# Performance work log

Hardware: AMD Instinct MI355X
Metric: run time of the kernel (lower is better)

Reference implementation:

```python
import jax, jax.numpy as jnp
import numpy as np


def lstm_cell(x, h, c, Wi, Wh, b):
    # PyTorch LSTMCell gate order: i, f, g, o
    g = x @ Wi.T + h @ Wh.T + b
    i, f, gg, o = jnp.split(g, 4, axis=-1)
    c = jax.nn.sigmoid(f) * c + jax.nn.sigmoid(i) * jnp.tanh(gg)
    h = jax.nn.sigmoid(o) * jnp.tanh(c)
    return h, c


def setup_inputs() -> dict:
    key = jax.random.key(0)
    ks = jax.random.split(key, 32)
    S, B, L, N, T = 20, 16, 30, 6, 20
    H, E, Vs, Vt = 512, 512, 50000, 30000
    w = lambda k, shape: jax.random.normal(k, shape, jnp.float32) * 0.05
    return {
        'articles': jax.random.randint(ks[0], (S, B, L), 0, Vs, jnp.int32),
        'summaries': jax.random.randint(ks[1], (N, B, T), 0, Vt, jnp.int32),
        'emb_src': w(ks[2], (Vs, E)),
        'emb_tgt': w(ks[3], (Vt, E)),
        'we_Wi': w(ks[4], (4 * H, E)), 'we_Wh': w(ks[5], (4 * H, H)), 'we_b': w(ks[6], (4 * H,)),
        'se_Wi': w(ks[7], (4 * H, H)), 'se_Wh': w(ks[8], (4 * H, H)), 'se_b': w(ks[9], (4 * H,)),
        'W_feat': w(ks[10], (H, H)), 'b_feat': w(ks[11], (H,)),
        'wd_Wi': w(ks[12], (4 * H, E)), 'wd_Wh': w(ks[13], (4 * H, H)), 'wd_b': w(ks[14], (4 * H,)),
        'W_vocab': w(ks[15], (Vt, H)), 'b_vocab': w(ks[16], (Vt,)),
        'sd_Wi': w(ks[17], (4 * H, H)), 'sd_Wh': w(ks[18], (4 * H, H)), 'sd_b': w(ks[19], (4 * H,)),
        'attn_Wh': w(ks[20], (H, H)), 'attn_wc': w(ks[21], (H,)), 'attn_v': w(ks[22], (H,)),
        'W_out': w(ks[23], (H, 2 * H)), 'b_out': w(ks[24], (H,)),
    }


def _forward(articles, summaries, emb_src, emb_tgt, we_Wi, we_Wh, we_b,
             se_Wi, se_Wh, se_b, W_feat, b_feat, wd_Wi, wd_Wh, wd_b,
             W_vocab, b_vocab, sd_Wi, sd_Wh, sd_b, attn_Wh, attn_wc, attn_v,
             W_out, b_out):
    S, B, L = articles.shape
    H = we_Wh.shape[1]

    # ---- word encoder: LSTMCell over each sentence, vmapped over S ----
    def encode_sentence(tokens):  # [B, L]
        x = emb_src[tokens]  # [B, L, E]
        z = jnp.zeros((B, H), x.dtype)
        def step(hc, xt):
            h, c = lstm_cell(xt, hc[0], hc[1], we_Wi, we_Wh, we_b)
            return (h, c), None
        (h, _), _ = jax.lax.scan(step, (z, z), jnp.swapaxes(x, 0, 1))
        return h
    word_hx = jax.vmap(encode_sentence)(articles)  # [S, B, H]

    # ---- sentence encoder: LSTM over sentence dim ----
    z = jnp.zeros((B, H), word_hx.dtype)
    def senc_step(hc, x):
        h, c = lstm_cell(x, hc[0], hc[1], se_Wi, se_Wh, se_b)
        return (h, c), h
    (s_hx, s_cx), sent_out = jax.lax.scan(senc_step, (z, z), word_hx)  # sent_out [S,B,H]
    sent_feat = sent_out @ W_feat.T + b_feat  # precomputed attention features

    mask = (articles[:, :, 0:1] > 0).astype(jnp.float32)  # [S, B, 1]
    coverage0 = jnp.zeros_like(mask)

    # ---- hierarchical decoder over summary sentences ----
    def sent_step(carry, sent):  # sent [B, T]
        w_hx, w_cx, s_hx, s_cx, coverage, loss = carry
        seq = sent.T  # [T, B]

        def word_step(wc, ba):
            wh, wcell, l = wc
            wb, wa = ba
            wh, wcell = lstm_cell(emb_tgt[wb], wh, wcell, wd_Wi, wd_Wh, wd_b)
            logits = wh @ W_vocab.T + b_vocab  # [B, V]
            logp = jax.nn.log_softmax(logits, axis=-1)
            nll = -jnp.take_along_axis(logp, wa[:, None], axis=1)[:, 0]
            m = (wa != 0).astype(logits.dtype)  # ignore_index=0
            l = l + jnp.sum(nll * m) / jnp.maximum(jnp.sum(m), 1.0)
            return (wh, wcell, l), None

        (w_hx, w_cx, loss), _ = jax.lax.scan(word_step, (w_hx, w_cx, loss), (seq[:-1], seq[1:]))

        # sentence decoder step with coverage attention over S sentences
        s_h2, s_cx = lstm_cell(w_hx, s_hx, s_cx, sd_Wi, sd_Wh, sd_b)
        e = jnp.einsum('sbh,h->sb', jnp.tanh(sent_feat + s_h2 @ attn_Wh.T + coverage * attn_wc), attn_v)
        e = jnp.where(mask[:, :, 0] > 0, e, -1e9)
        align = jax.nn.softmax(e, axis=0)[:, :, None]  # [S, B, 1]
        context = jnp.sum(align * sent_out, axis=0)  # [B, H]
        final = jnp.tanh(jnp.concatenate([context, s_h2], axis=-1) @ W_out.T + b_out)
        # coverage loss (with pre-update coverage), then accumulate coverage
        loss = loss + jnp.mean(jnp.sum(jnp.minimum(align[:, :, 0], coverage[:, :, 0]), axis=0))
        coverage = coverage + align
        return (final, w_cx, final, s_cx, coverage, loss), None

    init = (s_hx, s_cx, s_hx, s_cx, coverage0, jnp.float32(0.0))
    (_, _, _, _, _, loss), _ = jax.lax.scan(sent_step, init, summaries)
    return loss


def reference(articles, summaries, emb_src, emb_tgt, we_Wi, we_Wh, we_b,
              se_Wi, se_Wh, se_b, W_feat, b_feat, wd_Wi, wd_Wh, wd_b,
              W_vocab, b_vocab, sd_Wi, sd_Wh, sd_b, attn_Wh, attn_wc, attn_v,
              W_out, b_out):
    return _forward(articles, summaries, emb_src, emb_tgt, we_Wi, we_Wh, we_b,
                    se_Wi, se_Wh, se_b, W_feat, b_feat, wd_Wi, wd_Wh, wd_b,
                    W_vocab, b_vocab, sd_Wi, sd_Wh, sd_b, attn_Wh, attn_wc,
                    attn_v, W_out, b_out)
```

## Files before the change

### kernel.cpp

```cpp
#include <hip/hip_runtime.h>
#include <cstdint>
#include <cstddef>

#define H 512
#define SS 20
#define BB 16
#define LL 30
#define NN 6
#define TT 20
#define VT 30000
#define MROWS 1824
#define NSTEPS 114
#define MPAD 1856
#define NT2 120
#define UBLK 16
#define NV 232
#define MEGA 248

#define SCOPE_AGENT __HIP_MEMORY_SCOPE_AGENT

typedef __attribute__((ext_vector_type(8))) short bf16x8;
typedef __attribute__((ext_vector_type(4))) float f32x4;

__device__ __forceinline__ float sigmoidf_(float x) { return 1.f / (1.f + expf(-x)); }
__device__ __forceinline__ float b2f(ushort u) { return __uint_as_float(((uint32_t)u) << 16); }
__device__ __forceinline__ ushort f2b_rne(float f) {
  uint32_t u = __float_as_uint(f);
  return (ushort)((u + 0x7fffu + ((u >> 16) & 1u)) >> 16);
}

__device__ __forceinline__ void ast_u32(uint* p, uint v) {
  __hip_atomic_store(p, v, __ATOMIC_RELAXED, SCOPE_AGENT);
}
__device__ __forceinline__ uint ald_u32(const uint* p) {
  return __hip_atomic_load(p, __ATOMIC_RELAXED, SCOPE_AGENT);
}

__device__ __forceinline__ void sbar(uint* flags, int slot, int nblk, uint phase)
{
  __syncthreads();
  if (threadIdx.x == 0) {
    __builtin_amdgcn_fence(__ATOMIC_RELEASE, "agent");
    ast_u32(&flags[slot * 16], phase);
  }
  if ((int)threadIdx.x < nblk) {
    while (ald_u32(&flags[threadIdx.x * 16]) < phase)
      __builtin_amdgcn_s_sleep(1);
  }
  __syncthreads();
  if (threadIdx.x == 0)
    __builtin_amdgcn_fence(__ATOMIC_ACQUIRE, "agent");
  __syncthreads();
}

struct PrepP {
  const int* articles; const int* summaries;
  const float* emb_src; const float* emb_tgt;
  const float* we_Wi; const float* wd_Wi; const float* we_Wh;
  const float* se_Wi; const float* se_Wh; const float* W_feat;
  const float* wd_Wh; const float* sd_Wi; const float* sd_Wh;
  const float* attn_Wh; const float* W_out;
  ushort* A_we; ushort* A_wd;
  ushort* weWi; ushort* wdWi; ushort* weWh;
  ushort* seWi; ushort* seWh; ushort* wfeat;
  ushort* wdWh; ushort* sdWi; ushort* sdWh;
  ushort* attnWh; ushort* Wout;
};

__device__ __forceinline__ void conv_f2b(const float* __restrict__ src,
                                         ushort* __restrict__ dst, int n4,
                                         int t0, int stride)
{
  for (int i = t0; i < n4; i += stride) {
    float4 v = reinterpret_cast<const float4*>(src)[i];
    ushort4 o;
    o.x = f2b_rne(v.x); o.y = f2b_rne(v.y);
    o.z = f2b_rne(v.z); o.w = f2b_rne(v.w);
    reinterpret_cast<ushort4*>(dst)[i] = o;
  }
}

__global__ __launch_bounds__(256) void prep_kernel(PrepP P)
{
  const int t0 = blockIdx.x * 256 + threadIdx.x;
  const int stride = gridDim.x * 256;
  for (int i = t0; i < SS * BB * LL * H; i += stride) {
    int m = i >> 9, k = i & 511;
    int l = m / (SS * BB), sb = m % (SS * BB);
    int tok = P.articles[sb * LL + l];
    P.A_we[i] = f2b_rne(P.emb_src[(size_t)tok * H + k]);
  }
  for (int i = t0; i < MROWS * H; i += stride) {
    int m = i >> 9, k = i & 511;
    int stp = m >> 4, b = m & 15;
    int n = stp / (TT - 1), t = stp % (TT - 1);
    int tok = P.summaries[(n * BB + b) * TT + t];
    P.A_wd[i] = f2b_rne(P.emb_tgt[(size_t)tok * H + k]);
  }
  const int Q = 4 * H * H / 4;
  conv_f2b(P.we_Wi, P.weWi, Q, t0, stride);
  conv_f2b(P.wd_Wi, P.wdWi, Q, t0, stride);
  conv_f2b(P.we_Wh, P.weWh, Q, t0, stride);
  conv_f2b(P.se_Wi, P.seWi, Q, t0, stride);
  conv_f2b(P.se_Wh, P.seWh, Q, t0, stride);
  conv_f2b(P.wd_Wh, P.wdWh, Q, t0, stride);
  conv_f2b(P.sd_Wi, P.sdWi, Q, t0, stride);
  conv_f2b(P.sd_Wh, P.sdWh, Q, t0, stride);
  conv_f2b(P.W_feat, P.wfeat, H * H / 4, t0, stride);
  conv_f2b(P.attn_Wh, P.attnWh, H * H / 4, t0, stride);
  conv_f2b(P.W_out, P.Wout, H * 2 * H / 4, t0, stride);
}

__global__ __launch_bounds__(512) void proj_mfma_kernel(
    const ushort* __restrict__ A_we, const ushort* __restrict__ weWi,
    const float* __restrict__ we_b, ushort* __restrict__ XiW,
    const ushort* __restrict__ A_wd, const ushort* __restrict__ wdWi,
    const float* __restrict__ wd_b, ushort* __restrict__ XiD)
{
  int bid = blockIdx.x;
  const ushort* A; const ushort* W; const float* bias; ushort* C; int M, mt, nt;
  if (bid < 1200) { A = A_we; W = weWi; bias = we_b; C = XiW; M = 9600; mt = bid >> 3; nt = bid & 7; }
  else { int b2 = bid - 1200; A = A_wd; W = wdWi; bias = wd_b; C = XiD; M = MROWS; mt = b2 >> 3; nt = b2 & 7; }
  const int tid = threadIdx.x, wid = tid >> 6, lane = tid & 63;
  const int wm = wid >> 2, wn = wid & 3;
  const int m0 = mt * 64 + wm * 32, n0 = nt * 256 + wn * 64;
  const int lr = lane & 15, lk = (lane >> 4) << 3;

  f32x4 acc[2][4];
#pragma unroll
  for (int i = 0; i < 2; ++i)
#pragma unroll
    for (int nf = 0; nf < 4; ++nf) acc[i][nf] = (f32x4)0.0f;

  for (int k0 = 0; k0 < H; k0 += 32) {
    bf16x8 a[2], b[4];
#pragma unroll
    for (int i = 0; i < 2; ++i) {
      int m = m0 + i * 16 + lr;
      bf16x8 az = (bf16x8)(short)0;
      if (m < M) az = *reinterpret_cast<const bf16x8*>(A + (size_t)m * H + k0 + lk);
      a[i] = az;
    }
#pragma unroll
    for (int nf = 0; nf < 4; ++nf)
      b[nf] = *reinterpret_cast<const bf16x8*>(W + (size_t)(n0 + nf * 16 + lr) * H + k0 + lk);
#pragma unroll
    for (int i = 0; i < 2; ++i)
#pragma unroll
      for (int nf = 0; nf < 4; ++nf)
        acc[i][nf] = __builtin_amdgcn_mfma_f32_16x16x32_bf16(a[i], b[nf], acc[i][nf], 0, 0, 0);
  }
#pragma unroll
  for (int i = 0; i < 2; ++i)
#pragma unroll
    for (int nf = 0; nf < 4; ++nf) {
      int n = n0 + nf * 16 + lr;
      float bv = bias[n];
#pragma unroll
      for (int jreg = 0; jreg < 4; ++jreg) {
        int row = m0 + i * 16 + (lane >> 4) * 4 + jreg;
        if (row < M) C[(size_t)row * 2048 + n] = f2b_rne(acc[i][nf][jreg] + bv);
      }
    }
}

struct MP {
  const ushort* XiW; const ushort* XiD;
  const ushort* weWh; const ushort* seWi; const ushort* seWh;
  const ushort* wfeat; const ushort* wdWh; const ushort* sdWi;
  const ushort* sdWh; const ushort* attnWh; const ushort* Wout;
  const float* se_b; const float* b_feat; const float* sd_b; const float* b_out;
  const float* attn_wc; const float* attn_v; const int* articles;
  ushort* h0; ushort* h1;
  float* XiS;
  ushort* sh0; ushort* sh1;
  float* sent_out; ushort* sent_out_bf; float* sent_feat;
  ushort* wh_bf; ushort* sdh_bf; ushort* final_bf; ushort* catb;
  float* qb; float* loss;
  uint* sflags;
  uint* vbflags;
  uint* vflag;
  const float* Wv; ushort* Wv_bf; const float* bv; float* partials;
};

__global__ __launch_bounds__(512) void mega_kernel(MP P)
{
  const int tid = threadIdx.x, bid = blockIdx.x;
  const int wid = tid >> 6, lane = tid & 63;
  const int lr = lane & 15;
  const int lk = (lane >> 4) << 3;
  const int orow = (lane >> 4) << 2;

  const bool isSeq = (bid < 128) && ((bid & 7) == 0);

  if (!isSeq) {
    const int v = (bid < 128) ? (bid - (bid >> 3) - 1) : (bid - UBLK);
    const int mt = v >> 3, chunk = v & 7;
    __shared__ float red[4][64][2];

    if (tid == 0) {
      while (ald_u32(P.vflag) < 1u) __builtin_amdgcn_s_sleep(16);
    }
    __syncthreads();
    {
      const int n4 = VT * H / 4;
      for (int i = v * 512 + tid; i < n4; i += NV * 512) {
        float4 w = reinterpret_cast<const float4*>(P.Wv)[i];
        ushort4 o;
        o.x = f2b_rne(w.x); o.y = f2b_rne(w.y);
        o.z = f2b_rne(w.z); o.w = f2b_rne(w.w);
        reinterpret_cast<ushort4*>(P.Wv_bf)[i] = o;
      }
    }
    sbar(P.vbflags, v, NV, 1u);

    {
      int lastStep = mt * 4 + 3; if (lastStep > NSTEPS - 1) lastStep = NSTEPS - 1;
      uint want = 2u + (uint)(lastStep / (TT - 1));
      if (tid == 0) {
        while (ald_u32(P.vflag) < want) __builtin_amdgcn_s_sleep(16);
        __builtin_amdgcn_fence(__ATOMIC_ACQUIRE, "agent");
      }
      __syncthreads();
    }

    const int wm = wid >> 2, wn = wid & 3;
    const int m0 = mt * 64 + wm * 32;
    bf16x8 areg[2][16];
#pragma unroll
    for (int i = 0; i < 2; ++i)
#pragma unroll
      for (int kk = 0; kk < 16; ++kk)
        areg[i][kk] = *reinterpret_cast<const bf16x8*>(
            P.wh_bf + (size_t)(m0 + i * 16 + lr) * H + kk * 32 + lk);

    for (int nt2 = 0; nt2 < 15; ++nt2) {
      const int n0 = chunk * 3840 + nt2 * 256 + wn * 64;
      f32x4 acc[2][4];
#pragma unroll
      for (int i = 0; i < 2; ++i)
#pragma unroll
        for (int nf = 0; nf < 4; ++nf) acc[i][nf] = (f32x4)0.0f;

#pragma unroll 4
      for (int kk = 0; kk < 16; ++kk) {
        bf16x8 b[4];
#pragma unroll
        for (int nf = 0; nf < 4; ++nf) {
          int n = n0 + nf * 16 + lr;
          bf16x8 bz = (bf16x8)(short)0;
          if (n < VT) bz = *reinterpret_cast<const bf16x8*>(P.Wv_bf + (size_t)n * H + kk * 32 + lk);
          b[nf] = bz;
        }
#pragma unroll
        for (int i = 0; i < 2; ++i)
#pragma unroll
          for (int nf = 0; nf < 4; ++nf)
            acc[i][nf] = __builtin_amdgcn_mfma_f32_16x16x32_bf16(areg[i][kk], b[nf], acc[i][nf], 0, 0, 0);
      }

      float bc[4];
      int val[4];
#pragma unroll
      for (int nf = 0; nf < 4; ++nf) {
        int n = n0 + nf * 16 + lr;
        val[nf] = (n < VT);
        bc[nf] = val[nf] ? P.bv[n] : 0.f;
      }
#pragma unroll
      for (int i = 0; i < 2; ++i) {
#pragma unroll
        for (int jreg = 0; jreg < 4; ++jreg) {
          float lg[4];
          float mx = -3.0e38f;
#pragma unroll
          for (int nf = 0; nf < 4; ++nf) {
            lg[nf] = val[nf] ? (acc[i][nf][jreg] + bc[nf]) : -3.0e38f;
            mx = fmaxf(mx, lg[nf]);
          }
#pragma unroll
          for (int d = 1; d < 16; d <<= 1) mx = fmaxf(mx, __shfl_xor(mx, d));
          float s = 0.f;
#pragma unroll
          for (int nf = 0; nf < 4; ++nf) s += val[nf] ? expf(lg[nf] - mx) : 0.f;
#pragma unroll
          for (int d = 1; d < 16; d <<= 1) s += __shfl_xor(s, d);
          if (lr == 0) {
            int rloc = wm * 32 + i * 16 + (lane >> 4) * 4 + jreg;
            red[wn][rloc][0] = mx;
            red[wn][rloc][1] = s;
          }
        }
      }
      __syncthreads();
      if (tid < 64) {
        int r2 = tid;
        float M = -3.0e38f;
#pragma unroll
        for (int q = 0; q < 4; ++q) M = fmaxf(M, red[q][r2][0]);
        float S = 0.f;
#pragma unroll
        for (int q = 0; q < 4; ++q) S += red[q][r2][1] * expf(red[q][r2][0] - M);
        size_t p = ((size_t)(mt * 64 + r2) * NT2 + chunk * 15 + nt2) * 2;
        P.partials[p] = M;
        P.partials[p + 1] = S;
      }
      __syncthreads();
    }
    return;
  }

  const int sid = bid >> 3;
  __shared__ f32x4 hred[2][4][64];
  __shared__ float e_l[SS], align_l[SS], cov_l[SS];
  const int gw = sid * 8 + wid;
  uint ph = 0;

  {
    float cst[5][4];
#pragma unroll
    for (int it = 0; it < 5; ++it)
#pragma unroll
      for (int rg = 0; rg < 4; ++rg) cst[it][rg] = 0.f;
    ushort* cur = P.h0;
    ushort* nxt = P.h1;
    const int ug = gw & 31;
    const int unit = ug * 16 + lr;
    const ushort* wb = P.weWh + (size_t)(ug * 16 + lr) * H + lk;
    for (int l = 0; l < LL; ++l) {
#pragma unroll
      for (int it = 0; it < 5; ++it) {
        int mt = (gw + it * 128) >> 5;
        f32x4 acc[4];
#pragma unroll
        for (int g = 0; g < 4; ++g) acc[g] = (f32x4)0.0f;
        const ushort* ab = cur + (size_t)(mt * 16 + lr) * H + lk;
#pragma unroll
        for (int k0 = 0; k0 < H; k0 += 32) {
          bf16x8 a = *reinterpret_cast<const bf16x8*>(ab + k0);
#pragma unroll
          for (int g = 0; g < 4; ++g) {
            bf16x8 b = *reinterpret_cast<const bf16x8*>(wb + (size_t)g * H * H + k0);
            acc[g] = __builtin_amdgcn_mfma_f32_16x16x32_bf16(a, b, acc[g], 0, 0, 0);
          }
        }
#pragma unroll
        for (int rg = 0; rg < 4; ++rg) {
          int row = mt * 16 + orow + rg;
          const ushort* xi = P.XiW + (size_t)(l * 320 + row) * 2048 + unit;
          float gi = acc[0][rg] + b2f(xi[0]);
          float gf = acc[1][rg] + b2f(xi[512]);
          float gc = acc[2][rg] + b2f(xi[1024]);
          float go = acc[3][rg] + b2f(xi[1536]);
          float c = sigmoidf_(gf) * cst[it][rg] + sigmoidf_(gi) * tanhf(gc);
          float h = sigmoidf_(go) * tanhf(c);
          cst[it][rg] = c;
          nxt[(size_t)row * H + unit] = f2b_rne(h);
        }
      }
      sbar(P.sflags, sid, UBLK, ++ph);
      ushort* t = cur; cur = nxt; nxt = t;
    }
    {
      const ushort* wbs = P.seWi + (size_t)(ug * 16 + lr) * H + lk;
#pragma unroll
      for (int it = 0; it < 5; ++it) {
        int mt = (gw + it * 128) >> 5;
        f32x4 acc[4];
#pragma unroll
        for (int g = 0; g < 4; ++g) acc[g] = (f32x4)0.0f;
        const ushort* ab = cur + (size_t)(mt * 16 + lr) * H + lk;
#pragma unroll
        for (int k0 = 0; k0 < H; k0 += 32) {
          bf16x8 a = *reinterpret_cast<const bf16x8*>(ab + k0);
#pragma unroll
          for (int g = 0; g < 4; ++g) {
            bf16x8 b = *reinterpret_cast<const bf16x8*>(wbs + (size_t)g * H * H + k0);
            acc[g] = __builtin_amdgcn_mfma_f32_16x16x32_bf16(a, b, acc[g], 0, 0, 0);
          }
        }
#pragma unroll
        for (int rg = 0; rg < 4; ++rg) {
          int row = mt * 16 + orow + rg;
#pragma unroll
          for (int g = 0; g < 4; ++g)
            P.XiS[(size_t)row * 2048 + g * H + unit] = acc[g][rg] + P.se_b[g * H + unit];
        }
      }
    }
    sbar(P.sflags, sid, UBLK, ++ph);
    if (sid == 0 && tid == 0)
      __hip_atomic_store(P.vflag, 1u, __ATOMIC_RELEASE, SCOPE_AGENT);
  }

  float cw[4] = {0.f, 0.f, 0.f, 0.f};
  float csd[4] = {0.f, 0.f, 0.f, 0.f};
  {
    float cse[4] = {0.f, 0.f, 0.f, 0.f};
    ushort* cur = P.sh0;
    ushort* nxt = P.sh1;
    const int ug = sid * 2 + wid;
    const int unit = ug * 16 + lr;
    for (int s = 0; s < SS; ++s) {
      if (wid < 2) {
        f32x4 acc[4];
#pragma unroll
        for (int g = 0; g < 4; ++g) acc[g] = (f32x4)0.0f;
        const ushort* ab = cur + (size_t)lr * H + lk;
        const ushort* wb = P.seWh + (size_t)(ug * 16 + lr) * H + lk;
#pragma unroll
        for (int k0 = 0; k0 < H; k0 += 32) {
          bf16x8 a = *reinterpret_cast<const bf16x8*>(ab + k0);
#pragma unroll
          for (int g = 0; g < 4; ++g) {
            bf16x8 b = *reinterpret_cast<const bf16x8*>(wb + (size_t)g * H * H + k0);
            acc[g] = __builtin_amdgcn_mfma_f32_16x16x32_bf16(a, b, acc[g], 0, 0, 0);
          }
        }
#pragma unroll
        for (int rg = 0; rg < 4; ++rg) {
          int row = orow + rg;
          const float* xi = P.XiS + (size_t)(s * 16 + row) * 2048 + unit;
          float gi = acc[0][rg] + xi[0];
          float gf = acc[1][rg] + xi[512];
          float gc = acc[2][rg] + xi[1024];
          float go = acc[3][rg] + xi[1536];
          float c = sigmoidf_(gf) * cse[rg] + sigmoidf_(gi) * tanhf(gc);
          float h = sigmoidf_(go) * tanhf(c);
          cse[rg] = c;
          nxt[(size_t)row * H + unit] = f2b_rne(h);
          P.sent_out[(size_t)(s * 16 + row) * H + unit] = h;
          P.sent_out_bf[(size_t)(s * 16 + row) * H + unit] = f2b_rne(h);
        }
      }
      sbar(P.sflags, sid, UBLK, ++ph);
      ushort* t = cur; cur = nxt; nxt = t;
    }
    if (wid < 2) {
      f32x4 v; v[0] = cse[0]; v[1] = cse[1]; v[2] = cse[2]; v[3] = cse[3];
      hred[wid][0][lane] = v;
#pragma unroll
      for (int rg = 0; rg < 4; ++rg) csd[rg] = cse[rg];
    }
    __syncthreads();
    if (wid < 4 && !(wid & 1)) {
      f32x4 v = hred[wid >> 1][0][lane];
      cw[0] = v[0]; cw[1] = v[1]; cw[2] = v[2]; cw[3] = v[3];
    }
    __syncthreads();
  }

  {
    const int ug = gw & 31;
    const int unit = ug * 16 + lr;
    const ushort* wb = P.wfeat + (size_t)(ug * 16 + lr) * H + lk;
#pragma unroll
    for (int it = 0; it < 5; ++it) {
      int mt = (gw + it * 128) >> 5;
      f32x4 acc = (f32x4)0.0f;
      const ushort* ab = P.sent_out_bf + (size_t)(mt * 16 + lr) * H + lk;
#pragma unroll
      for (int k0 = 0; k0 < H; k0 += 32) {
        bf16x8 a = *reinterpret_cast<const bf16x8*>(ab + k0);
        bf16x8 b = *reinterpret_cast<const bf16x8*>(wb + k0);
        acc = __builtin_amdgcn_mfma_f32_16x16x32_bf16(a, b, acc, 0, 0, 0);
      }
#pragma unroll
      for (int rg = 0; rg < 4; ++rg) {
        int row = mt * 16 + orow + rg;
        P.sent_feat[(size_t)row * H + unit] = acc[rg] + P.b_feat[unit];
      }
    }
    if (tid < SS) cov_l[tid] = 0.f;
    sbar(P.sflags, sid, UBLK, ++ph);
  }

  {
    const int half = wid & 1;
    const int ug2 = sid * 2 + (wid >> 1);
    const int unit2 = ug2 * 16 + lr;
    const int ug = sid * 2 + wid;
    const int unit = ug * 16 + lr;
    const int b_ = sid;

    for (int n = 0; n < NN; ++n) {
      bf16x8 wreg[4][8];
      if (wid < 4) {
#pragma unroll
        for (int g = 0; g < 4; ++g)
#pragma unroll
          for (int kk = 0; kk < 8; ++kk)
            wreg[g][kk] = *reinterpret_cast<const bf16x8*>(
                P.wdWh + (size_t)g * H * H + (size_t)(ug2 * 16 + lr) * H +
                half * 256 + kk * 32 + lk);
      }
      for (int t = 0; t < TT - 1; ++t) {
        int stp = n * (TT - 1) + t;
        f32x4 acc[4];
        if (wid < 4) {
          const ushort* A = (t == 0)
              ? ((n == 0) ? P.sh0 : P.final_bf)
              : P.wh_bf + (size_t)(stp - 1) * 16 * H;
#pragma unroll
          for (int g = 0; g < 4; ++g) acc[g] = (f32x4)0.0f;
          const ushort* ab = A + (size_t)lr * H + half * 256 + lk;
#pragma unroll
          for (int kk = 0; kk < 8; ++kk) {
            bf16x8 a = *reinterpret_cast<const bf16x8*>(ab + kk * 32);
#pragma unroll
            for (int g = 0; g < 4; ++g)
              acc[g] = __builtin_amdgcn_mfma_f32_16x16x32_bf16(a, wreg[g][kk], acc[g], 0, 0, 0);
          }
          if (half) {
#pragma unroll
            for (int g = 0; g < 4; ++g) hred[wid >> 1][g][lane] = acc[g];
          }
        }
        __syncthreads();
        if (wid < 4 && !half) {
#pragma unroll
          for (int g = 0; g < 4; ++g) acc[g] += hred[wid >> 1][g][lane];
#pragma unroll
          for (int rg = 0; rg < 4; ++rg) {
            int row = orow + rg;
            const ushort* xi = P.XiD + (size_t)(stp * 16 + row) * 2048 + unit2;
            float gi = acc[0][rg] + b2f(xi[0]);
            float gf = acc[1][rg] + b2f(xi[512]);
            float gc = acc[2][rg] + b2f(xi[1024]);
            float go = acc[3][rg] + b2f(xi[1536]);
            float c = sigmoidf_(gf) * cw[rg] + sigmoidf_(gi) * tanhf(gc);
            float h = sigmoidf_(go) * tanhf(c);
            cw[rg] = c;
            P.wh_bf[(size_t)(stp * 16 + row) * H + unit2] = f2b_rne(h);
          }
        }
        sbar(P.sflags, sid, UBLK, ++ph);
      }
      if (sid == 0 && tid == 0)
        __hip_atomic_store(P.vflag, 2u + (uint)n, __ATOMIC_RELEASE, SCOPE_AGENT);
      if (wid < 2) {
        f32x4 acc[4];
#pragma unroll
        for (int g = 0; g < 4; ++g) acc[g] = (f32x4)0.0f;
        const ushort* A1 = P.wh_bf + (size_t)(n * (TT - 1) + TT - 2) * 16 * H;
        const ushort* A2 = (n == 0) ? P.sh0 : P.final_bf;
        const ushort* ab1 = A1 + (size_t)lr * H + lk;
        const ushort* wb1 = P.sdWi + (size_t)(ug * 16 + lr) * H + lk;
#pragma unroll
        for (int k0 = 0; k0 < H; k0 += 32) {
          bf16x8 a = *reinterpret_cast<const bf16x8*>(ab1 + k0);
#pragma unroll
          for (int g = 0; g < 4; ++g) {
            bf16x8 b = *reinterpret_cast<const bf16x8*>(wb1 + (size_t)g * H * H + k0);
            acc[g] = __builtin_amdgcn_mfma_f32_16x16x32_bf16(a, b, acc[g], 0, 0, 0);
          }
        }
        const ushort* ab2 = A2 + (size_t)lr * H + lk;
        const ushort* wb2 = P.sdWh + (size_t)(ug * 16 + lr) * H + lk;
#pragma unroll
        for (int k0 = 0; k0 < H; k0 += 32) {
          bf16x8 a = *reinterpret_cast<const bf16x8*>(ab2 + k0);
#pragma unroll
          for (int g = 0; g < 4; ++g) {
            bf16x8 b = *reinterpret_cast<const bf16x8*>(wb2 + (size_t)g * H * H + k0);
            acc[g] = __builtin_amdgcn_mfma_f32_16x16x32_bf16(a, b, acc[g], 0, 0, 0);
          }
        }
#pragma unroll
        for (int rg = 0; rg < 4; ++rg) {
          int row = orow + rg;
          float gi = acc[0][rg] + P.sd_b[0 * H + unit];
          float gf = acc[1][rg] + P.sd_b[1 * H + unit];
          float gc = acc[2][rg] + P.sd_b[2 * H + unit];
          float go = acc[3][rg] + P.sd_b[3 * H + unit];
          float c = sigmoidf_(gf) * csd[rg] + sigmoidf_(gi) * tanhf(gc);
          float h = sigmoidf_(go) * tanhf(c);
          csd[rg] = c;
          P.sdh_bf[(size_t)row * H + unit] = f2b_rne(h);
        }
      }
      sbar(P.sflags, sid, UBLK, ++ph);
      if (wid < 2) {
        f32x4 acc = (f32x4)0.0f;
        const ushort* ab = P.sdh_bf + (size_t)lr * H + lk;
        const ushort* wb = P.attnWh + (size_t)(ug * 16 + lr) * H + lk;
#pragma unroll
        for (int k0 = 0; k0 < H; k0 += 32) {
          bf16x8 a = *reinterpret_cast<const bf16x8*>(ab + k0);
          bf16x8 b = *reinterpret_cast<const bf16x8*>(wb + k0);
          acc = __builtin_amdgcn_mfma_f32_16x16x32_bf16(a, b, acc, 0, 0, 0);
        }
#pragma unroll
        for (int rg = 0; rg < 4; ++rg)
          P.qb[(size_t)(orow + rg) * H + unit] = acc[rg];
      }
      sbar(P.sflags, sid, UBLK, ++ph);
      for (int s = wid; s < SS; s += 8) {
        float cov = cov_l[s];
        float sum = 0.f;
        for (int h2 = lane; h2 < H; h2 += 64)
          sum += tanhf(P.sent_feat[(size_t)(s * 16 + b_) * H + h2] +
                       P.qb[b_ * H + h2] + cov * P.attn_wc[h2]) * P.attn_v[h2];
#pragma unroll
        for (int d = 1; d < 64; d <<= 1) sum += __shfl_xor(sum, d);
        if (lane == 0)
          e_l[s] = (P.articles[(s * 16 + b_) * LL] > 0) ? sum : -1e9f;
      }
      __syncthreads();
      if (wid == 0) {
        float ev = (lane < SS) ? e_l[lane] : -3.0e38f;
        float mx = ev;
#pragma unroll
        for (int d = 1; d < 64; d <<= 1) mx = fmaxf(mx, __shfl_xor(mx, d));
        float ex = (lane < SS) ? expf(ev - mx) : 0.f;
        float s = ex;
#pragma unroll
        for (int d = 1; d < 64; d <<= 1) s += __shfl_xor(s, d);
        float al = ex / s;
        float cl = 0.f;
        if (lane < SS) {
          float cov = cov_l[lane];
          cl = fminf(al, cov);
          cov_l[lane] = cov + al;
          align_l[lane] = al;
        }
#pragma unroll
        for (int d = 1; d < 64; d <<= 1) cl += __shfl_xor(cl, d);
        if (lane == 0) atomicAdd(P.loss, cl * (1.f / BB));
      }
      __syncthreads();
      if (tid < 512) {
        float s = 0.f;
#pragma unroll
        for (int ss2 = 0; ss2 < SS; ++ss2)
          s += align_l[ss2] * P.sent_out[(size_t)(ss2 * 16 + b_) * H + tid];
        P.catb[b_ * 1024 + tid] = f2b_rne(s);
        P.catb[b_ * 1024 + 512 + tid] = P.sdh_bf[(size_t)b_ * H + tid];
      }
      sbar(P.sflags, sid, UBLK, ++ph);
      if (wid < 2) {
        f32x4 acc = (f32x4)0.0f;
        const ushort* ab = P.catb + (size_t)lr * 1024 + lk;
        const ushort* wb = P.Wout + (size_t)(ug * 16 + lr) * 1024 + lk;
#pragma unroll
        for (int k0 = 0; k0 < 1024; k0 += 32) {
          bf16x8 a = *reinterpret_cast<const bf16x8*>(ab + k0);
          bf16x8 b = *reinterpret_cast<const bf16x8*>(wb + k0);
          acc = __builtin_amdgcn_mfma_f32_16x16x32_bf16(a, b, acc, 0, 0, 0);
        }
#pragma unroll
        for (int rg = 0; rg < 4; ++rg) {
          int row = orow + rg;
          float v = tanhf(acc[rg] + P.b_out[unit]);
          P.final_bf[(size_t)row * H + unit] = f2b_rne(v);
        }
      }
      sbar(P.sflags, sid, UBLK, ++ph);
    }
    if (sid == 0 && tid == 0)
      __hip_atomic_store(P.vflag, 7u, __ATOMIC_RELEASE, SCOPE_AGENT);
  }
}

__global__ void tlog_kernel(const ushort* __restrict__ wh_bf,
                            const ushort* __restrict__ Wv_bf,
                            const float* __restrict__ bv,
                            const int* __restrict__ summaries,
                            float* __restrict__ tlog)
{
  int row = blockIdx.x;
  int lane = threadIdx.x;
  int b = row & 15, stp = row >> 4;
  int n = stp / (TT - 1), t = stp % (TT - 1);
  int tgt = summaries[(n * BB + b) * TT + t + 1];
  float s = 0.f;
  for (int k = lane; k < H; k += 64)
    s += b2f(wh_bf[(size_t)row * H + k]) * b2f(Wv_bf[(size_t)tgt * H + k]);
#pragma unroll
  for (int d = 1; d < 64; d <<= 1) s += __shfl_xor(s, d);
  if (lane == 0) tlog[row] = s + bv[tgt];
}

__global__ __launch_bounds__(256) void nll_kernel(
    const float* __restrict__ partials, const float* __restrict__ tlog,
    const int* __restrict__ summaries, float* __restrict__ loss)
{
  int stp = blockIdx.x;
  int tid = threadIdx.x;
  int rr = tid >> 4, ch = tid & 15;
  int row = stp * 16 + rr;
  const float* pr = partials + (size_t)row * NT2 * 2;
  float mx = -3.0e38f;
  for (int t2 = ch; t2 < NT2; t2 += 16) mx = fmaxf(mx, pr[t2 * 2]);
#pragma unroll
  for (int d = 1; d < 16; d <<= 1) mx = fmaxf(mx, __shfl_xor(mx, d));
  float s = 0.f;
  for (int t2 = ch; t2 < NT2; t2 += 16) s += pr[t2 * 2 + 1] * expf(pr[t2 * 2] - mx);
#pragma unroll
  for (int d = 1; d < 16; d <<= 1) s += __shfl_xor(s, d);
  __shared__ float sh_n[16], sh_m[16];
  if (ch == 0) {
    float lse = mx + logf(s);
    float nll = lse - tlog[row];
    int b = row & 15;
    int n = stp / (TT - 1), t = stp % (TT - 1);
    int wa = summaries[(n * BB + b) * TT + t + 1];
    sh_n[rr] = (wa != 0) ? nll : 0.f;
    sh_m[rr] = (wa != 0) ? 1.f : 0.f;
  }
  __syncthreads();
  if (tid == 0) {
    float sn = 0.f, sm = 0.f;
    for (int r2 = 0; r2 < 16; ++r2) { sn += sh_n[r2]; sm += sh_m[r2]; }
    atomicAdd(loss, sn / fmaxf(sm, 1.f));
  }
}

extern "C" void kernel_launch(void* const* d_in, const int* in_sizes, int n_in,
                              void* d_out, int out_size, void* d_ws, size_t ws_size,
                              hipStream_t stream)
{
  (void)in_sizes; (void)n_in; (void)out_size; (void)ws_size;
  const int*   articles  = (const int*)d_in[0];
  const int*   summaries = (const int*)d_in[1];
  const float* emb_src   = (const float*)d_in[2];
  const float* emb_tgt   = (const float*)d_in[3];
  const float* we_Wi = (const float*)d_in[4];
  const float* we_Wh = (const float*)d_in[5];
  const float* we_b  = (const float*)d_in[6];
  const float* se_Wi = (const float*)d_in[7];
  const float* se_Wh = (const float*)d_in[8];
  const float* se_b  = (const float*)d_in[9];
  const float* W_feat = (const float*)d_in[10];
  const float* b_feat = (const float*)d_in[11];
  const float* wd_Wi = (const float*)d_in[12];
  const float* wd_Wh = (const float*)d_in[13];
  const float* wd_b  = (const float*)d_in[14];
  const float* W_vocab = (const float*)d_in[15];
  const float* b_vocab = (const float*)d_in[16];
  const float* sd_Wi = (const float*)d_in[17];
  const float* sd_Wh = (const float*)d_in[18];
  const float* sd_b  = (const float*)d_in[19];
  const float* attn_Wh = (const float*)d_in[20];
  const float* attn_wc = (const float*)d_in[21];
  const float* attn_v  = (const float*)d_in[22];
  const float* W_out = (const float*)d_in[23];
  const float* b_out = (const float*)d_in[24];

  char* wsb = (char*)d_ws;
  size_t off = 0;
  auto alloc = [&](size_t bytes) -> char* {
    char* p = wsb + off;
    off += (bytes + 255) & ~(size_t)255;
    return p;
  };

  char* regA = alloc(9830400);
  ushort* A_we     = (ushort*)regA;
  ushort* wh_bf    = (ushort*)regA;
  float*  partials = (float*)(regA + 1900544);
  float*  tlogb    = (float*)(regA + 3682304);

  ushort* A_wd = (ushort*)alloc((size_t)MROWS * H * 2);

  char* regW = alloc((size_t)9600 * 2048 * 2);
  ushort* XiW   = (ushort*)regW;
  ushort* Wv_bf = (ushort*)regW;

  ushort* XiD = (ushort*)alloc((size_t)MROWS * 2048 * 2);

  ushort* weWi  = (ushort*)alloc(4 * H * H * 2);
  ushort* wdWi  = (ushort*)alloc(4 * H * H * 2);
  ushort* weWh  = (ushort*)alloc(4 * H * H * 2);
  ushort* seWi  = (ushort*)alloc(4 * H * H * 2);
  ushort* seWh  = (ushort*)alloc(4 * H * H * 2);
  ushort* wdWh  = (ushort*)alloc(4 * H * H * 2);
  ushort* sdWi  = (ushort*)alloc(4 * H * H * 2);
  ushort* sdWh  = (ushort*)alloc(4 * H * H * 2);
  ushort* wfeat = (ushort*)alloc(H * H * 2);
  ushort* attnWh= (ushort*)alloc(H * H * 2);
  ushort* Wout  = (ushort*)alloc(H * 2 * H * 2);

  float*  XiS = (float*)alloc((size_t)320 * 2048 * 4);
  ushort* h0  = (ushort*)alloc(320 * H * 2);
  ushort* h1  = (ushort*)alloc(320 * H * 2);
  ushort* sh0 = (ushort*)alloc(16 * H * 2);
  ushort* sh1 = (ushort*)alloc(16 * H * 2);
  float*  sent_out    = (float*)alloc(320 * H * 4);
  ushort* sent_out_bf = (ushort*)alloc(320 * H * 2);
  float*  sent_feat   = (float*)alloc(320 * H * 4);
  ushort* sdh_bf   = (ushort*)alloc(16 * H * 2);
  ushort* final_bf = (ushort*)alloc(16 * H * 2);
  ushort* catb     = (ushort*)alloc(16 * 1024 * 2);
  float*  qb       = (float*)alloc(16 * H * 4);
  uint*   sflags  = (uint*)alloc(UBLK * 16 * 4);
  uint*   vbflags = (uint*)alloc(NV * 16 * 4);
  uint*   vflag   = (uint*)alloc(256);

  float* loss = (float*)d_out;
  hipMemsetAsync(loss, 0, 4, stream);
  hipMemsetAsync(h0, 0, 320 * H * 2, stream);
  hipMemsetAsync(sh0, 0, 16 * H * 2, stream);
  hipMemsetAsync(sflags, 0, UBLK * 16 * 4, stream);
  hipMemsetAsync(vbflags, 0, NV * 16 * 4, stream);
  hipMemsetAsync(vflag, 0, 256, stream);

  {
    PrepP P = {articles, summaries, emb_src, emb_tgt,
               we_Wi, wd_Wi, we_Wh, se_Wi, se_Wh, W_feat,
               wd_Wh, sd_Wi, sd_Wh, attn_Wh, W_out,
               A_we, A_wd, weWi, wdWi, weWh, seWi, seWh, wfeat,
               wdWh, sdWi, sdWh, attnWh, Wout};
    prep_kernel<<<2048, 256, 0, stream>>>(P);
  }

  proj_mfma_kernel<<<1432, 512, 0, stream>>>(A_we, weWi, we_b, XiW,
                                             A_wd, wdWi, wd_b, XiD);

  hipMemsetAsync((char*)wh_bf + (size_t)MROWS * H * 2, 0,
                 (size_t)(MPAD - MROWS) * H * 2, stream);

  {
    MP P;
    P.XiW = XiW; P.XiD = XiD;
    P.weWh = weWh; P.seWi = seWi; P.seWh = seWh; P.wfeat = wfeat;
    P.wdWh = wdWh; P.sdWi = sdWi; P.sdWh = sdWh; P.attnWh = attnWh; P.Wout = Wout;
    P.se_b = se_b; P.b_feat = b_feat; P.sd_b = sd_b; P.b_out = b_out;
    P.attn_wc = attn_wc; P.attn_v = attn_v; P.articles = articles;
    P.h0 = h0; P.h1 = h1; P.XiS = XiS; P.sh0 = sh0; P.sh1 = sh1;
    P.sent_out = sent_out; P.sent_out_bf = sent_out_bf; P.sent_feat = sent_feat;
    P.wh_bf = wh_bf; P.sdh_bf = sdh_bf; P.final_bf = final_bf; P.catb = catb;
    P.qb = qb; P.loss = loss;
    P.sflags = sflags; P.vbflags = vbflags; P.vflag = vflag;
    P.Wv = W_vocab; P.Wv_bf = Wv_bf; P.bv = b_vocab; P.partials = partials;
    mega_kernel<<<MEGA, 512, 0, stream>>>(P);
  }

  tlog_kernel<<<MROWS, 64, 0, stream>>>(wh_bf, Wv_bf, b_vocab, summaries, tlogb);
  nll_kernel<<<NSTEPS, 256, 0, stream>>>(partials, tlogb, summaries, loss);
}
```

Measured before the change: 5.429 ms.

## Compute attention query per block locally, dropping a grid barrier; remap sequential blocks

Each sequential block now computes its own batch row's attention query (sdh · attnWh) with a scalar dot-product loop into shared memory. Before, the query was produced by distributed MFMA across blocks into a global buffer, followed by a cross-block barrier. This removes one grid-wide software barrier per decoder step and the global qb round trip. In exchange each block reads the whole attn_Wh matrix with scalar FMAs. Sequential blocks are also remapped from every eighth block among the first 128 to the first 16 block IDs, with vocab-projection workers taking the rest.

```diff
diff --git a/kernel.cpp b/kernel.cpp
--- a/kernel.cpp
+++ b/kernel.cpp
@@ -176,10 +176,10 @@
   ushort* sh0; ushort* sh1;
   float* sent_out; ushort* sent_out_bf; float* sent_feat;
   ushort* wh_bf; ushort* sdh_bf; ushort* final_bf; ushort* catb;
-  float* qb; float* loss;
+  float* loss;
   uint* sflags;
+  uint* vflag;
   uint* vbflags;
-  uint* vflag;
   const float* Wv; ushort* Wv_bf; const float* bv; float* partials;
 };
 
@@ -191,10 +191,8 @@
   const int lk = (lane >> 4) << 3;
   const int orow = (lane >> 4) << 2;
 
-  const bool isSeq = (bid < 128) && ((bid & 7) == 0);
-
-  if (!isSeq) {
-    const int v = (bid < 128) ? (bid - (bid >> 3) - 1) : (bid - UBLK);
+  if (bid >= UBLK) {
+    const int v = bid - UBLK;
     const int mt = v >> 3, chunk = v & 7;
     __shared__ float red[4][64][2];
 
@@ -310,10 +308,12 @@
     return;
   }
 
-  const int sid = bid >> 3;
   __shared__ f32x4 hred[2][4][64];
   __shared__ float e_l[SS], align_l[SS], cov_l[SS];
-  const int gw = sid * 8 + wid;
+  __shared__ float qb_l[H];
+  __shared__ ushort sdh_l[H];
+  const int gw = bid * 8 + wid;
+  const int b_ = bid;
   uint ph = 0;
 
   {
@@ -358,7 +358,7 @@
           nxt[(size_t)row * H + unit] = f2b_rne(h);
         }
       }
-      sbar(P.sflags, sid, UBLK, ++ph);
+      sbar(P.sflags, bid, UBLK, ++ph);
       ushort* t = cur; cur = nxt; nxt = t;
     }
     {
@@ -388,8 +388,8 @@
         }
       }
     }
-    sbar(P.sflags, sid, UBLK, ++ph);
-    if (sid == 0 && tid == 0)
+    sbar(P.sflags, bid, UBLK, ++ph);
+    if (bid == 0 && tid == 0)
       __hip_atomic_store(P.vflag, 1u, __ATOMIC_RELEASE, SCOPE_AGENT);
   }
 
@@ -399,7 +399,7 @@
     float cse[4] = {0.f, 0.f, 0.f, 0.f};
     ushort* cur = P.sh0;
     ushort* nxt = P.sh1;
-    const int ug = sid * 2 + wid;
+    const int ug = bid * 2 + wid;
     const int unit = ug * 16 + lr;
     for (int s = 0; s < SS; ++s) {
       if (wid < 2) {
@@ -433,7 +433,7 @@
           P.sent_out_bf[(size_t)(s * 16 + row) * H + unit] = f2b_rne(h);
         }
       }
-      sbar(P.sflags, sid, UBLK, ++ph);
+      sbar(P.sflags, bid, UBLK, ++ph);
       ushort* t = cur; cur = nxt; nxt = t;
     }
     if (wid < 2) {
@@ -472,16 +472,15 @@
       }
     }
     if (tid < SS) cov_l[tid] = 0.f;
-    sbar(P.sflags, sid, UBLK, ++ph);
+    sbar(P.sflags, bid, UBLK, ++ph);
   }
 
   {
     const int half = wid & 1;
-    const int ug2 = sid * 2 + (wid >> 1);
+    const int ug2 = bid * 2 + (wid >> 1);
     const int unit2 = ug2 * 16 + lr;
-    const int ug = sid * 2 + wid;
+    const int ug = bid * 2 + wid;
     const int unit = ug * 16 + lr;
-    const int b_ = sid;
 
     for (int n = 0; n < NN; ++n) {
       bf16x8 wreg[4][8];
@@ -534,9 +533,9 @@
             P.wh_bf[(size_t)(stp * 16 + row) * H + unit2] = f2b_rne(h);
           }
         }
-        sbar(P.sflags, sid, UBLK, ++ph);
-      }
-      if (sid == 0 && tid == 0)
+        sbar(P.sflags, bid, UBLK, ++ph);
+      }
+      if (bid == 0 && tid == 0)
         __hip_atomic_store(P.vflag, 2u + (uint)n, __ATOMIC_RELEASE, SCOPE_AGENT);
       if (wid < 2) {
         f32x4 acc[4];
@@ -579,28 +578,32 @@
           P.sdh_bf[(size_t)row * H + unit] = f2b_rne(h);
         }
       }
-      sbar(P.sflags, sid, UBLK, ++ph);
-      if (wid < 2) {
-        f32x4 acc = (f32x4)0.0f;
-        const ushort* ab = P.sdh_bf + (size_t)lr * H + lk;
-        const ushort* wb = P.attnWh + (size_t)(ug * 16 + lr) * H + lk;
-#pragma unroll
-        for (int k0 = 0; k0 < H; k0 += 32) {
-          bf16x8 a = *reinterpret_cast<const bf16x8*>(ab + k0);
-          bf16x8 b = *reinterpret_cast<const bf16x8*>(wb + k0);
-          acc = __builtin_amdgcn_mfma_f32_16x16x32_bf16(a, b, acc, 0, 0, 0);
-        }
-#pragma unroll
-        for (int rg = 0; rg < 4; ++rg)
-          P.qb[(size_t)(orow + rg) * H + unit] = acc[rg];
-      }
-      sbar(P.sflags, sid, UBLK, ++ph);
+      sbar(P.sflags, bid, UBLK, ++ph);
+      if (tid < 256)
+        reinterpret_cast<uint*>(sdh_l)[tid] =
+            reinterpret_cast<const uint*>(P.sdh_bf + (size_t)b_ * H)[tid];
+      __syncthreads();
+      {
+        int u = tid;
+        float s = 0.f;
+        const ushort* wr = P.attnWh + (size_t)u * H;
+#pragma unroll 4
+        for (int k0 = 0; k0 < H; k0 += 8) {
+          bf16x8 w8 = *reinterpret_cast<const bf16x8*>(wr + k0);
+          bf16x8 h8 = *reinterpret_cast<const bf16x8*>(sdh_l + k0);
+#pragma unroll
+          for (int j = 0; j < 8; ++j)
+            s += b2f((ushort)h8[j]) * b2f((ushort)w8[j]);
+        }
+        qb_l[u] = s;
+      }
+      __syncthreads();
       for (int s = wid; s < SS; s += 8) {
         float cov = cov_l[s];
         float sum = 0.f;
         for (int h2 = lane; h2 < H; h2 += 64)
           sum += tanhf(P.sent_feat[(size_t)(s * 16 + b_) * H + h2] +
-                       P.qb[b_ * H + h2] + cov * P.attn_wc[h2]) * P.attn_v[h2];
+                       qb_l[h2] + cov * P.attn_wc[h2]) * P.attn_v[h2];
 #pragma unroll
         for (int d = 1; d < 64; d <<= 1) sum += __shfl_xor(sum, d);
         if (lane == 0)
@@ -629,15 +632,15 @@
         if (lane == 0) atomicAdd(P.loss, cl * (1.f / BB));
       }
       __syncthreads();
-      if (tid < 512) {
+      {
         float s = 0.f;
 #pragma unroll
         for (int ss2 = 0; ss2 < SS; ++ss2)
           s += align_l[ss2] * P.sent_out[(size_t)(ss2 * 16 + b_) * H + tid];
         P.catb[b_ * 1024 + tid] = f2b_rne(s);
-        P.catb[b_ * 1024 + 512 + tid] = P.sdh_bf[(size_t)b_ * H + tid];
-      }
-      sbar(P.sflags, sid, UBLK, ++ph);
+        P.catb[b_ * 1024 + 512 + tid] = sdh_l[tid];
+      }
+      sbar(P.sflags, bid, UBLK, ++ph);
       if (wid < 2) {
         f32x4 acc = (f32x4)0.0f;
         const ushort* ab = P.catb + (size_t)lr * 1024 + lk;
@@ -655,9 +658,9 @@
           P.final_bf[(size_t)row * H + unit] = f2b_rne(v);
         }
       }
-      sbar(P.sflags, sid, UBLK, ++ph);
-    }
-    if (sid == 0 && tid == 0)
+      sbar(P.sflags, bid, UBLK, ++ph);
+    }
+    if (bid == 0 && tid == 0)
       __hip_atomic_store(P.vflag, 7u, __ATOMIC_RELEASE, SCOPE_AGENT);
   }
 }
@@ -792,7 +795,6 @@
   ushort* sdh_bf   = (ushort*)alloc(16 * H * 2);
   ushort* final_bf = (ushort*)alloc(16 * H * 2);
   ushort* catb     = (ushort*)alloc(16 * 1024 * 2);
-  float*  qb       = (float*)alloc(16 * H * 4);
   uint*   sflags  = (uint*)alloc(UBLK * 16 * 4);
   uint*   vbflags = (uint*)alloc(NV * 16 * 4);
   uint*   vflag   = (uint*)alloc(256);
@@ -830,8 +832,8 @@
     P.h0 = h0; P.h1 = h1; P.XiS = XiS; P.sh0 = sh0; P.sh1 = sh1;
     P.sent_out = sent_out; P.sent_out_bf = sent_out_bf; P.sent_feat = sent_feat;
     P.wh_bf = wh_bf; P.sdh_bf = sdh_bf; P.final_bf = final_bf; P.catb = catb;
-    P.qb = qb; P.loss = loss;
-    P.sflags = sflags; P.vbflags = vbflags; P.vflag = vflag;
+    P.loss = loss;
+    P.sflags = sflags; P.vflag = vflag; P.vbflags = vbflags;
     P.Wv = W_vocab; P.Wv_bf = Wv_bf; P.bv = b_vocab; P.partials = partials;
     mega_kernel<<<MEGA, 512, 0, stream>>>(P);
   }
```

Result: faster. 5.067 ms (-6.7%).
